# Kernel tuning notes

Hardware: AMD Instinct MI355X
Metric: run time of the kernel (lower is better)

Reference implementation:

```python
import jax, jax.numpy as jnp
import numpy as np

NUM_EMBEDDINGS = 8192
EMBEDDING_DIM = 256
COMMITMENT_COST = 0.25


def setup_inputs() -> dict:
    key = jax.random.key(0)
    k1, k2 = jax.random.split(key)
    hidden_states = jax.random.normal(k1, (16, EMBEDDING_DIM, 32, 32), dtype=jnp.float32)
    # nn.Embedding weight init: uniform(-1/K, 1/K)
    codebook = jax.random.uniform(
        k2, (NUM_EMBEDDINGS, EMBEDDING_DIM), dtype=jnp.float32,
        minval=-1.0 / NUM_EMBEDDINGS, maxval=1.0 / NUM_EMBEDDINGS)
    return {"hidden_states": hidden_states, "codebook": codebook}


def reference(hidden_states, codebook):
    B, C, H, W = hidden_states.shape
    x = jnp.transpose(hidden_states, (0, 2, 3, 1))  # BHWC
    flat = x.reshape(-1, C)                          # [N, D]
    # squared L2 distances: ||f||^2 - 2 f.e + ||e||^2  -> [N, K]
    distances = (jnp.sum(flat * flat, axis=1, keepdims=True)
                 - 2.0 * flat @ codebook.T
                 + jnp.sum(codebook * codebook, axis=1))
    indices = jnp.argmin(distances, axis=1)          # [N]
    # one-hot @ codebook is mathematically a gather:
    quantized = codebook[indices].reshape(x.shape)   # BHWC
    # vq loss (stop_gradient mirrors .detach(); values identical in fwd)
    e_loss = jnp.mean((jax.lax.stop_gradient(quantized) - x) ** 2)
    q_loss = jnp.mean((quantized - jax.lax.stop_gradient(x)) ** 2)
    vq_loss = q_loss + COMMITMENT_COST * e_loss
    # straight-through estimator
    quantized = x + jax.lax.stop_gradient(quantized - x)
    quantized = jnp.transpose(quantized, (0, 3, 1, 2))  # back to NCHW
    indices = indices.reshape(B, -1)
    return quantized, indices, vq_loss
```

## Files before the change

kernel.cpp:

```cpp
#include <hip/hip_runtime.h>
#include <hip/hip_bf16.h>
#include <stdint.h>

#define NROWS 16384
#define KCODES 8192
#define DIM 256
#define HW 1024
#define CHW (DIM*HW)
#define IDX_OFF 4194304
#define LOSS_OFF 4210688
#define TAU 1.2e-4f

typedef unsigned long long u64;
typedef unsigned int u32;
typedef unsigned short ushort_t;

using frag = __attribute__((ext_vector_type(8))) short;
using accf = __attribute__((ext_vector_type(4))) float;

__device__ __forceinline__ u32 forder(float f) {
    u32 u = __float_as_uint(f);
    return (u & 0x80000000u) ? ~u : (u | 0x80000000u);
}
__device__ __forceinline__ float unforder(u32 v) {
    u32 u = (v & 0x80000000u) ? (v ^ 0x80000000u) : ~v;
    return __uint_as_float(u);
}
__device__ __forceinline__ ushort_t bf16bits(float v) {
    __hip_bfloat16 t = __float2bfloat16(v);
    return *reinterpret_cast<ushort_t*>(&t);
}
__device__ __forceinline__ float bflo(u32 u) { return __uint_as_float(u << 16); }
__device__ __forceinline__ float bfhi(u32 u) { return __uint_as_float(u & 0xFFFF0000u); }
__device__ __forceinline__ void async_cp16(const uint4* gp, uint4* lp) {
    __builtin_amdgcn_global_load_lds(
        (const __attribute__((address_space(1))) unsigned int*)gp,
        (__attribute__((address_space(3))) unsigned int*)lp, 16, 0, 0);
}

__device__ __forceinline__ float max_dpp16(float v) {
    int x;
    x = __builtin_amdgcn_update_dpp(__float_as_int(v), __float_as_int(v), 0xB1, 0xF, 0xF, true);
    v = fmaxf(v, __int_as_float(x));
    x = __builtin_amdgcn_update_dpp(__float_as_int(v), __float_as_int(v), 0x4E, 0xF, 0xF, true);
    v = fmaxf(v, __int_as_float(x));
    x = __builtin_amdgcn_update_dpp(__float_as_int(v), __float_as_int(v), 0x124, 0xF, 0xF, true);
    v = fmaxf(v, __int_as_float(x));
    x = __builtin_amdgcn_update_dpp(__float_as_int(v), __float_as_int(v), 0x128, 0xF, 0xF, true);
    v = fmaxf(v, __int_as_float(x));
    return v;
}

__device__ __forceinline__ u64 exact_key(const float* __restrict__ cb,
                                         const float* __restrict__ fs,
                                         float rn_row, int code) {
    const float4* e4 = reinterpret_cast<const float4*>(&cb[(size_t)code << 8]);
    float acc = 0.0f;
    #pragma unroll 16
    for (int kk = 0; kk < 64; ++kk) {
        float4 ev = e4[kk];
        float4 fv = *reinterpret_cast<const float4*>(&fs[kk << 2]);
        acc = fmaf(fv.x, ev.x, acc);
        acc = fmaf(fv.y, ev.y, acc);
        acc = fmaf(fv.z, ev.z, acc);
        acc = fmaf(fv.w, ev.w, acc);
    }
    float s = __fadd_rn(rn_row, -2.0f * acc);
    return ((u64)forder(s) << 32) | (u64)code;
}


__global__ __launch_bounds__(64)
void convert_hs(const float* __restrict__ hs, ushort_t* __restrict__ Abf,
                float* __restrict__ rn, u32* __restrict__ rowmin,
                float* __restrict__ out) {
    __shared__ uint4 tile[64 * 17];
    const int t = threadIdx.x;
    const int row0 = blockIdx.x * 64;
    const int row = row0 + t;
    rowmin[row] = 0xFFFFFFFFu;
    if (row == 0) out[LOSS_OFF] = 0.0f;
    const int b = row >> 10, hw = row & 1023;
    const float* p = hs + (size_t)b * CHW + hw;
    uint4* Abf4 = reinterpret_cast<uint4*>(Abf);
    float halfsum[2];
    #pragma unroll
    for (int h = 0; h < 2; ++h) {
        float r[8];
        for (int i = 0; i < 128; i += 8) {
            ushort_t pk[8];
            #pragma unroll
            for (int j = 0; j < 8; ++j) {
                int c = h * 128 + i + j;
                float v = p[(size_t)c * HW];
                pk[j] = bf16bits(v);
                float sq = __fmul_rn(v, v);
                r[j] = (i == 0) ? sq : __fadd_rn(r[j], sq);
            }
            uint4 o;
            o.x = (u32)pk[0] | ((u32)pk[1] << 16);
            o.y = (u32)pk[2] | ((u32)pk[3] << 16);
            o.z = (u32)pk[4] | ((u32)pk[5] << 16);
            o.w = (u32)pk[6] | ((u32)pk[7] << 16);
            tile[t * 17 + (i >> 3)] = o;
        }
        halfsum[h] = __fadd_rn(__fadd_rn(__fadd_rn(r[0], r[1]), __fadd_rn(r[2], r[3])),
                               __fadd_rn(__fadd_rn(r[4], r[5]), __fadd_rn(r[6], r[7])));
        __syncthreads();
        #pragma unroll
        for (int pass = 0; pass < 16; ++pass) {
            int rr = pass * 4 + (t >> 4);
            int uh = t & 15;
            uint4 v = tile[rr * 17 + uh];
            int orow = row0 + rr;
            int u = h * 16 + uh;
            int g = u >> 3;
            int slot = (u & 7) ^ (orow & 7);
            Abf4[(size_t)g * 131072 + (size_t)orow * 8 + slot] = v;
        }
        __syncthreads();
    }
    rn[row] = __fadd_rn(halfsum[0], halfsum[1]);
}

__global__ __launch_bounds__(256)
void convert_cb(const float* __restrict__ cb, ushort_t* __restrict__ Bbf) {
    int o = blockIdx.x * 256 + threadIdx.x;
    int g = o >> 16;
    int rem = o & 65535;
    int code = rem >> 3;
    int slot = rem & 7;
    int u = slot ^ (code & 7);
    const float4* src = reinterpret_cast<const float4*>(
        cb + (size_t)code * DIM + (size_t)(g * 8 + u) * 8);
    float4 v0 = src[0], v1 = src[1];
    uint4 out_v;
    out_v.x = (u32)bf16bits(v0.x) | ((u32)bf16bits(v0.y) << 16);
    out_v.y = (u32)bf16bits(v0.z) | ((u32)bf16bits(v0.w) << 16);
    out_v.z = (u32)bf16bits(v1.x) | ((u32)bf16bits(v1.y) << 16);
    out_v.w = (u32)bf16bits(v1.z) | ((u32)bf16bits(v1.w) << 16);
    reinterpret_cast<uint4*>(Bbf)[o] = out_v;
}

__global__ __launch_bounds__(1024, 4)
void mfma_approx(const ushort_t* __restrict__ Abf, const ushort_t* __restrict__ Bbf,
                 float* __restrict__ sbmin, u32* __restrict__ rowmin) {
    __shared__ uint4 As4[2][2048];
    __shared__ uint4 Bs4[2][2048];

    const int tid = threadIdx.x;
    const int n0 = blockIdx.x << 8;
    const int c0 = blockIdx.y << 8;
    const int w = tid >> 6, L = tid & 63;
    const int wr = w & 3, wc = w >> 2;
    const int m = L & 15, q = L >> 4;
    const uint4* gA = reinterpret_cast<const uint4*>(Abf);
    const uint4* gB = reinterpret_cast<const uint4*>(Bbf);

    accf acc[4][4];
    #pragma unroll
    for (int rt = 0; rt < 4; ++rt)
        #pragma unroll
        for (int ct = 0; ct < 4; ++ct) acc[rt][ct] = (accf){0.f, 0.f, 0.f, 0.f};

#define STAGE(buf, gg) do {                                                   \
    _Pragma("unroll")                                                         \
    for (int r_ = 0; r_ < 2; ++r_) {                                          \
        int j_ = (r_ << 10) + tid;                                            \
        async_cp16(gA + ((size_t)(gg) * 131072 + (size_t)n0 * 8 + j_),        \
                   &As4[buf][j_]);                                            \
    }                                                                         \
    _Pragma("unroll")                                                         \
    for (int r_ = 0; r_ < 2; ++r_) {                                          \
        int j_ = (r_ << 10) + tid;                                            \
        async_cp16(gB + ((size_t)(gg) * 65536 + (size_t)c0 * 8 + j_),         \
                   &Bs4[buf][j_]);                                            \
    }                                                                         \
} while (0)

    STAGE(0, 0);
    __syncthreads();

    #pragma unroll
    for (int g = 0; g < 4; ++g) {
        const int cur = g & 1;
        if (g < 3) STAGE(cur ^ 1, g + 1);
        #pragma unroll
        for (int ks = 0; ks < 2; ++ks) {
            const int us = ((ks << 2) + q) ^ (m & 7);
            frag a[4];
            #pragma unroll
            for (int rt = 0; rt < 4; ++rt)
                a[rt] = *reinterpret_cast<const frag*>(
                    &As4[cur][((wr << 6) + (rt << 4) + m) * 8 + us]);
            #pragma unroll
            for (int ct = 0; ct < 4; ++ct) {
                frag bfr = *reinterpret_cast<const frag*>(
                    &Bs4[cur][((wc << 6) + (ct << 4) + m) * 8 + us]);
                #pragma unroll
                for (int rt = 0; rt < 4; ++rt)
                    acc[rt][ct] = __builtin_amdgcn_mfma_f32_16x16x32_bf16(a[rt], bfr, acc[rt][ct], 0, 0, 0);
            }
        }
        if (g < 3) __syncthreads();
    }
#undef STAGE

    const int cbase = (blockIdx.y << 3) + (wc << 1);
    #pragma unroll
    for (int rt = 0; rt < 4; ++rt) {
        #pragma unroll
        for (int reg = 0; reg < 4; ++reg) {
            float mx[2];
            #pragma unroll
            for (int p = 0; p < 2; ++p)
                mx[p] = fmaxf(acc[rt][2 * p][reg], acc[rt][2 * p + 1][reg]);
            #pragma unroll
            for (int p = 0; p < 2; ++p) mx[p] = max_dpp16(mx[p]);
            if (m == 0) {
                int row = n0 + (wr << 6) + (rt << 4) + (q << 2) + reg;
                float mn[2];
                #pragma unroll
                for (int p = 0; p < 2; ++p) {
                    mn[p] = -2.0f * mx[p];
                    sbmin[(size_t)row * 256 + cbase + p] = mn[p];
                }
                float m2 = fminf(mn[0], mn[1]);
                atomicMin(&rowmin[row], forder(m2));
            }
        }
    }
}

__global__ __launch_bounds__(64, 4)
void rescore(const float* __restrict__ hs, const float* __restrict__ cb,
             const float* __restrict__ rn, const float* __restrict__ sbmin,
             const u32* __restrict__ rowmin, u64* __restrict__ keys,
             const ushort_t* __restrict__ Bbf) {
    __shared__ __align__(16) float fs[256];
    __shared__ int list[256];
    __shared__ int surv[512];
    __shared__ int cnt, cnt2;
    const int bid = blockIdx.x;
    const int row = ((bid & 7) << 11) + (bid >> 3);
    const int l = threadIdx.x;
    if (l == 0) { cnt = 0; cnt2 = 0; }
    const int b = row >> 10, hw = row & 1023;
    const float* hp = hs + (size_t)b * CHW + hw;
    #pragma unroll
    for (int j = 0; j < 4; ++j) fs[l + 64 * j] = hp[(size_t)(l + 64 * j) * HW];
    __syncthreads();

    float thr = unforder(rowmin[row]) + TAU;
    #pragma unroll
    for (int j = 0; j < 4; ++j) {
        int sb = l + 64 * j;
        if (sbmin[(size_t)row * 256 + sb] <= thr) {
            int pos = atomicAdd(&cnt, 1);
            list[pos] = sb;
        }
    }
    __syncthreads();
    const int C = cnt;
    const float rn_row = rn[row];
    const uint4* gB4 = reinterpret_cast<const uint4*>(Bbf);
    u64 best = ~0ull;

    const int cid = l >> 3, kp = l & 7;
    float4 freg4[8];
    #pragma unroll
    for (int j = 0; j < 8; ++j)
        freg4[j] = *reinterpret_cast<const float4*>(&fs[kp * 32 + 4 * j]);

    const uint4* gBp = gB4 + (size_t)(kp >> 1) * 65536;
    for (int it = 0; it < C * 4; ++it) {
        int code = list[it >> 2] * 32 + (it & 3) * 8 + cid;
        const int cx = code & 7, cbase8 = code << 3;
        uint4 bv[4];
        #pragma unroll
        for (int j = 0; j < 4; ++j) {
            int u = ((kp & 1) << 2) + j;
            bv[j] = gBp[cbase8 + (u ^ cx)];
        }
        float f0 = 0.f, f1 = 0.f, f2 = 0.f, f3 = 0.f;
        #pragma unroll
        for (int j = 0; j < 4; ++j) {
            float4 fa = freg4[2 * j];
            float4 fb = freg4[2 * j + 1];
            f0 = fmaf(fa.x, bflo(bv[j].x), f0);
            f1 = fmaf(fa.y, bfhi(bv[j].x), f1);
            f2 = fmaf(fa.z, bflo(bv[j].y), f2);
            f3 = fmaf(fa.w, bfhi(bv[j].y), f3);
            f0 = fmaf(fb.x, bflo(bv[j].z), f0);
            f1 = fmaf(fb.y, bfhi(bv[j].z), f1);
            f2 = fmaf(fb.z, bflo(bv[j].w), f2);
            f3 = fmaf(fb.w, bfhi(bv[j].w), f3);
        }
        float f = (f0 + f1) + (f2 + f3);
        f += __shfl_xor(f, 1, 64);
        f += __shfl_xor(f, 2, 64);
        f += __shfl_xor(f, 4, 64);
        if (kp == 0 && -2.0f * f <= thr) {
            int pos = atomicAdd(&cnt2, 1);
            if (pos < 512) surv[pos] = code;
            else {
                u64 key = exact_key(cb, fs, rn_row, code);
                if (key < best) best = key;
            }
        }
    }
    __syncthreads();
    const int S = (cnt2 < 512) ? cnt2 : 512;
    for (int s0 = l; s0 < S; s0 += 64) {
        u64 key = exact_key(cb, fs, rn_row, surv[s0]);
        if (key < best) best = key;
    }
    #pragma unroll
    for (int sh = 1; sh < 64; sh <<= 1) {
        u64 o = __shfl_xor(best, sh, 64);
        if (o < best) best = o;
    }
    if (l == 0) keys[row] = best;
}

__global__ __launch_bounds__(256)
void gather_kernel(const float* __restrict__ hs, const float* __restrict__ cb,
                   const u64* __restrict__ keys, float* __restrict__ out) {
    __shared__ int codes_s[32];
    __shared__ float q_s[32][257];
    __shared__ float red[4];
    const int g = blockIdx.x;
    const int b = g >> 5;
    const int hw0 = (g & 31) << 5;
    const int t = threadIdx.x;
    const int nbase = b * HW + hw0;

    if (t < 32) {
        int code = (int)(keys[nbase + t] & 0xFFFFFFFFULL);
        codes_s[t] = code;
        out[IDX_OFF + nbase + t] = (float)code;
    }
    __syncthreads();

    const int r = t >> 3, f4 = t & 7;
    const float4* crow = reinterpret_cast<const float4*>(cb + (size_t)codes_s[r] * DIM);
    #pragma unroll
    for (int j = 0; j < 8; ++j) {
        float4 v = crow[f4 + 8 * j];
        *reinterpret_cast<float4*>(&q_s[r][4 * (f4 + 8 * j)]) = v;
    }
    __syncthreads();

    float d2 = 0.0f;
    const int hw = t & 31, cof = t >> 5;
    #pragma unroll 8
    for (int it = 0; it < 32; ++it) {
        int c = it * 8 + cof;
        size_t off = (size_t)b * CHW + (size_t)c * HW + hw0 + hw;
        float x = hs[off];
        float qv = q_s[hw][c];
        out[off] = x + (qv - x);
        float d = qv - x;
        d2 = fmaf(d, d, d2);
    }
    #pragma unroll
    for (int sh = 32; sh >= 1; sh >>= 1) d2 += __shfl_xor(d2, sh, 64);
    if ((t & 63) == 0) red[t >> 6] = d2;
    __syncthreads();
    if (t == 0) {
        float tot = red[0] + red[1] + red[2] + red[3];
        atomicAdd(out + LOSS_OFF, tot * (1.25f / 4194304.0f));
    }
}

extern "C" void kernel_launch(void* const* d_in, const int* in_sizes, int n_in,
                              void* d_out, int out_size, void* d_ws, size_t ws_size,
                              hipStream_t stream) {
    const float* hs = (const float*)d_in[0];
    const float* cb = (const float*)d_in[1];
    float* out = (float*)d_out;
    char* ws = (char*)d_ws;
    u64*      keys   = (u64*)(ws + 0);
    float*    rn     = (float*)(ws + 131072);
    u32*      rowmin = (u32*)(ws + 196608);
    ushort_t* Abf    = (ushort_t*)(ws + 262144);
    ushort_t* Bbf    = (ushort_t*)(ws + 8650752);
    float*    sbmin  = (float*)(ws + 12845056);

    convert_hs<<<NROWS / 64, 64, 0, stream>>>(hs, Abf, rn, rowmin, out);
    convert_cb<<<1024, 256, 0, stream>>>(cb, Bbf);
    mfma_approx<<<dim3(NROWS / 256, KCODES / 256), 1024, 0, stream>>>(Abf, Bbf, sbmin, rowmin);
    rescore<<<NROWS, 64, 0, stream>>>(hs, cb, rn, sbmin, rowmin, keys, Bbf);
    gather_kernel<<<512, 256, 0, stream>>>(hs, cb, keys, out);
}
```

Measured before the change: 260.4 us.

## Widen convert_hs and gather grids, prefetch codebook rows in rescore

convert_hs now runs 128 threads per block, so the two channel halves are converted in parallel instead of one after the other, and the half-sums are combined through shared memory. The rescore loop loads the next candidate's bf16 codebook fragments before computing the current dot product, to hide global-load latency at the cost of more registers. gather_kernel is split four ways over channels, giving 2048 smaller blocks with less shared memory each, to raise occupancy and parallelism. The index output is written only by the first channel slice, and each slice adds its own part of the loss atomically.

```diff
diff --git a/kernel.cpp b/kernel.cpp
--- a/kernel.cpp
+++ b/kernel.cpp
@@ -70,57 +70,60 @@
 }
 
 
-__global__ __launch_bounds__(64)
+__global__ __launch_bounds__(128)
 void convert_hs(const float* __restrict__ hs, ushort_t* __restrict__ Abf,
                 float* __restrict__ rn, u32* __restrict__ rowmin,
                 float* __restrict__ out) {
-    __shared__ uint4 tile[64 * 17];
+    __shared__ uint4 tile[2][64 * 17];
+    __shared__ float hsx[2][64];
     const int t = threadIdx.x;
+    const int tr = t & 63;
+    const int h = t >> 6;
     const int row0 = blockIdx.x * 64;
-    const int row = row0 + t;
-    rowmin[row] = 0xFFFFFFFFu;
-    if (row == 0) out[LOSS_OFF] = 0.0f;
+    const int row = row0 + tr;
+    if (h == 0) {
+        rowmin[row] = 0xFFFFFFFFu;
+        if (row == 0) out[LOSS_OFF] = 0.0f;
+    }
     const int b = row >> 10, hw = row & 1023;
     const float* p = hs + (size_t)b * CHW + hw;
     uint4* Abf4 = reinterpret_cast<uint4*>(Abf);
-    float halfsum[2];
-    #pragma unroll
-    for (int h = 0; h < 2; ++h) {
-        float r[8];
-        for (int i = 0; i < 128; i += 8) {
-            ushort_t pk[8];
-            #pragma unroll
-            for (int j = 0; j < 8; ++j) {
-                int c = h * 128 + i + j;
-                float v = p[(size_t)c * HW];
-                pk[j] = bf16bits(v);
-                float sq = __fmul_rn(v, v);
-                r[j] = (i == 0) ? sq : __fadd_rn(r[j], sq);
-            }
-            uint4 o;
-            o.x = (u32)pk[0] | ((u32)pk[1] << 16);
-            o.y = (u32)pk[2] | ((u32)pk[3] << 16);
-            o.z = (u32)pk[4] | ((u32)pk[5] << 16);
-            o.w = (u32)pk[6] | ((u32)pk[7] << 16);
-            tile[t * 17 + (i >> 3)] = o;
-        }
-        halfsum[h] = __fadd_rn(__fadd_rn(__fadd_rn(r[0], r[1]), __fadd_rn(r[2], r[3])),
-                               __fadd_rn(__fadd_rn(r[4], r[5]), __fadd_rn(r[6], r[7])));
-        __syncthreads();
-        #pragma unroll
-        for (int pass = 0; pass < 16; ++pass) {
-            int rr = pass * 4 + (t >> 4);
-            int uh = t & 15;
-            uint4 v = tile[rr * 17 + uh];
-            int orow = row0 + rr;
-            int u = h * 16 + uh;
-            int g = u >> 3;
-            int slot = (u & 7) ^ (orow & 7);
-            Abf4[(size_t)g * 131072 + (size_t)orow * 8 + slot] = v;
-        }
-        __syncthreads();
-    }
-    rn[row] = __fadd_rn(halfsum[0], halfsum[1]);
+
+    float r[8];
+    for (int i = 0; i < 128; i += 8) {
+        ushort_t pk[8];
+        #pragma unroll
+        for (int j = 0; j < 8; ++j) {
+            int c = h * 128 + i + j;
+            float v = p[(size_t)c * HW];
+            pk[j] = bf16bits(v);
+            float sq = __fmul_rn(v, v);
+            r[j] = (i == 0) ? sq : __fadd_rn(r[j], sq);
+        }
+        uint4 o;
+        o.x = (u32)pk[0] | ((u32)pk[1] << 16);
+        o.y = (u32)pk[2] | ((u32)pk[3] << 16);
+        o.z = (u32)pk[4] | ((u32)pk[5] << 16);
+        o.w = (u32)pk[6] | ((u32)pk[7] << 16);
+        tile[h][tr * 17 + (i >> 3)] = o;
+    }
+    float halfsum = __fadd_rn(__fadd_rn(__fadd_rn(r[0], r[1]), __fadd_rn(r[2], r[3])),
+                              __fadd_rn(__fadd_rn(r[4], r[5]), __fadd_rn(r[6], r[7])));
+    hsx[h][tr] = halfsum;
+    __syncthreads();
+
+    #pragma unroll
+    for (int pass = 0; pass < 16; ++pass) {
+        int rr = pass * 4 + (tr >> 4);
+        int uh = tr & 15;
+        uint4 v = tile[h][rr * 17 + uh];
+        int orow = row0 + rr;
+        int u = h * 16 + uh;
+        int g = u >> 3;
+        int slot = (u & 7) ^ (orow & 7);
+        Abf4[(size_t)g * 131072 + (size_t)orow * 8 + slot] = v;
+    }
+    if (h == 0) rn[row] = __fadd_rn(hsx[0][tr], hsx[1][tr]);
 }
 
 __global__ __launch_bounds__(256)
@@ -273,14 +276,32 @@
         freg4[j] = *reinterpret_cast<const float4*>(&fs[kp * 32 + 4 * j]);
 
     const uint4* gBp = gB4 + (size_t)(kp >> 1) * 65536;
-    for (int it = 0; it < C * 4; ++it) {
-        int code = list[it >> 2] * 32 + (it & 3) * 8 + cid;
-        const int cx = code & 7, cbase8 = code << 3;
-        uint4 bv[4];
+    const int NP = C * 4;
+    uint4 bv[4];
+    int code_cur = 0;
+    if (NP > 0) {
+        code_cur = list[0] * 32 + cid;
+        const int cx = code_cur & 7, cb8 = code_cur << 3;
         #pragma unroll
         for (int j = 0; j < 4; ++j) {
             int u = ((kp & 1) << 2) + j;
-            bv[j] = gBp[cbase8 + (u ^ cx)];
+            bv[j] = gBp[cb8 + (u ^ cx)];
+        }
+    }
+    for (int it = 0; it < NP; ++it) {
+        const int code = code_cur;
+        uint4 nv[4];
+        int code_nxt = 0;
+        const bool more = (it + 1 < NP);
+        if (more) {
+            int it2 = it + 1;
+            code_nxt = list[it2 >> 2] * 32 + (it2 & 3) * 8 + cid;
+            const int cx = code_nxt & 7, cb8 = code_nxt << 3;
+            #pragma unroll
+            for (int j = 0; j < 4; ++j) {
+                int u = ((kp & 1) << 2) + j;
+                nv[j] = gBp[cb8 + (u ^ cx)];
+            }
         }
         float f0 = 0.f, f1 = 0.f, f2 = 0.f, f3 = 0.f;
         #pragma unroll
@@ -308,6 +329,11 @@
                 if (key < best) best = key;
             }
         }
+        if (more) {
+            #pragma unroll
+            for (int j = 0; j < 4; ++j) bv[j] = nv[j];
+            code_cur = code_nxt;
+        }
     }
     __syncthreads();
     const int S = (cnt2 < 512) ? cnt2 : 512;
@@ -327,25 +353,28 @@
 void gather_kernel(const float* __restrict__ hs, const float* __restrict__ cb,
                    const u64* __restrict__ keys, float* __restrict__ out) {
     __shared__ int codes_s[32];
-    __shared__ float q_s[32][257];
+    __shared__ float q_s[32][65];
     __shared__ float red[4];
     const int g = blockIdx.x;
-    const int b = g >> 5;
-    const int hw0 = (g & 31) << 5;
+    const int b = g >> 7;
+    const int hw0 = ((g >> 2) & 31) << 5;
+    const int cz = g & 3;
+    const int c0g = cz << 6;
     const int t = threadIdx.x;
     const int nbase = b * HW + hw0;
 
     if (t < 32) {
         int code = (int)(keys[nbase + t] & 0xFFFFFFFFULL);
         codes_s[t] = code;
-        out[IDX_OFF + nbase + t] = (float)code;
+        if (cz == 0) out[IDX_OFF + nbase + t] = (float)code;
     }
     __syncthreads();
 
     const int r = t >> 3, f4 = t & 7;
-    const float4* crow = reinterpret_cast<const float4*>(cb + (size_t)codes_s[r] * DIM);
-    #pragma unroll
-    for (int j = 0; j < 8; ++j) {
+    const float4* crow = reinterpret_cast<const float4*>(
+        cb + (size_t)codes_s[r] * DIM + c0g);
+    #pragma unroll
+    for (int j = 0; j < 2; ++j) {
         float4 v = crow[f4 + 8 * j];
         *reinterpret_cast<float4*>(&q_s[r][4 * (f4 + 8 * j)]) = v;
     }
@@ -354,9 +383,9 @@
     float d2 = 0.0f;
     const int hw = t & 31, cof = t >> 5;
     #pragma unroll 8
-    for (int it = 0; it < 32; ++it) {
+    for (int it = 0; it < 8; ++it) {
         int c = it * 8 + cof;
-        size_t off = (size_t)b * CHW + (size_t)c * HW + hw0 + hw;
+        size_t off = (size_t)b * CHW + (size_t)(c0g + c) * HW + hw0 + hw;
         float x = hs[off];
         float qv = q_s[hw][c];
         out[off] = x + (qv - x);
@@ -387,9 +416,9 @@
     ushort_t* Bbf    = (ushort_t*)(ws + 8650752);
     float*    sbmin  = (float*)(ws + 12845056);
 
-    convert_hs<<<NROWS / 64, 64, 0, stream>>>(hs, Abf, rn, rowmin, out);
+    convert_hs<<<NROWS / 64, 128, 0, stream>>>(hs, Abf, rn, rowmin, out);
     convert_cb<<<1024, 256, 0, stream>>>(cb, Bbf);
     mfma_approx<<<dim3(NROWS / 256, KCODES / 256), 1024, 0, stream>>>(Abf, Bbf, sbmin, rowmin);
     rescore<<<NROWS, 64, 0, stream>>>(hs, cb, rn, sbmin, rowmin, keys, Bbf);
-    gather_kernel<<<512, 256, 0, stream>>>(hs, cb, keys, out);
-}
+    gather_kernel<<<2048, 256, 0, stream>>>(hs, cb, keys, out);
+}
```

Measured after the change: 275.2 us. 1.06x slower.
